# Kernel optimization log

Hardware: AMD Instinct MI355X
Metric: run time of the kernel (lower is better)

Reference implementation:

```python
import jax, jax.numpy as jnp
import numpy as np

VOCAB = 50000
D = 512          # in_feat == word_embedding_dim
B = 4096
S = 128
NUM_LABELS = 3


def setup_inputs() -> dict:
    key = jax.random.key(0)
    ks = jax.random.split(key, 16)
    ids_a = jax.random.randint(ks[0], (B, S), 0, VOCAB, dtype=jnp.int32)
    ids_b = jax.random.randint(ks[1], (B, S), 0, VOCAB, dtype=jnp.int32)
    mask_a = jax.random.randint(ks[2], (B, S), 0, 2) > 0
    mask_b = jax.random.randint(ks[3], (B, S), 0, 2) > 0
    s = 0.02
    W_emb = jax.random.normal(ks[4], (VOCAB, D), jnp.float32) * s
    W_emb = W_emb.at[0].set(0.0)  # padding_idx=0
    enc_w1 = jax.random.normal(ks[5], (D, D), jnp.float32) * s
    enc_b1 = jnp.zeros((D,), jnp.float32)
    enc_w2 = jax.random.normal(ks[6], (D, D), jnp.float32) * s
    enc_b2 = jnp.zeros((D,), jnp.float32)
    cls_w1 = jax.random.normal(ks[7], (2 * D, D), jnp.float32) * s
    cls_b1 = jnp.zeros((D,), jnp.float32)
    cls_w2 = jax.random.normal(ks[8], (D, NUM_LABELS), jnp.float32) * s
    cls_b2 = jnp.zeros((NUM_LABELS,), jnp.float32)
    return {
        "text_a_inputs_id": ids_a, "text_b_inputs_id": ids_b,
        "text_a_attention_mask": mask_a, "text_b_attention_mask": mask_b,
        "W_emb": W_emb,
        "enc_w1": enc_w1, "enc_b1": enc_b1, "enc_w2": enc_w2, "enc_b2": enc_b2,
        "cls_w1": cls_w1, "cls_b1": cls_b1, "cls_w2": cls_w2, "cls_b2": cls_b2,
    }


def _encode(ids, mask, W_emb, w1, b1, w2, b2):
    # embedding gather [B,S,D], fused masked sum-pool -> [B,D]
    emb = W_emb[ids]
    pooled = jnp.einsum("bsd,bs->bd", emb, mask.astype(emb.dtype))
    x = jnp.tanh(pooled @ w1 + b1)
    x = jnp.tanh(x @ w2 + b2)  # dropout is identity in eval
    return x


def reference(text_a_inputs_id, text_b_inputs_id, text_a_attention_mask,
              text_b_attention_mask, W_emb, enc_w1, enc_b1, enc_w2, enc_b2,
              cls_w1, cls_b1, cls_w2, cls_b2):
    va = _encode(text_a_inputs_id, text_a_attention_mask, W_emb, enc_w1, enc_b1, enc_w2, enc_b2)
    vb = _encode(text_b_inputs_id, text_b_attention_mask, W_emb, enc_w1, enc_b1, enc_w2, enc_b2)
    pooled = jnp.concatenate([va, vb], axis=-1)  # [B, 2D]
    h = jnp.tanh(pooled @ cls_w1 + cls_b1)
    logits = h @ cls_w2 + cls_b2  # [B, num_labels]
    return logits
```

## Files before the change

kernel.cpp:

```cpp
#include <hip/hip_runtime.h>


typedef unsigned short u16;
typedef __attribute__((ext_vector_type(8))) short short8;
typedef __attribute__((ext_vector_type(4))) float f32x4;

__device__ __forceinline__ float bfu2f(u16 u) {
    union { unsigned int i; float f; } v;
    v.i = ((unsigned int)u) << 16;
    return v.f;
}

__device__ __forceinline__ u16 f2bfu(float f) {
    union { float f; unsigned int i; } v;
    v.f = f;
    unsigned int x = v.i;
    x += 0x7fffu + ((x >> 16) & 1u);
    return (u16)(x >> 16);
}

__device__ __forceinline__ int detect_wave(const u16* __restrict__ W,
                                           const unsigned int* __restrict__ m,
                                           int lane)
{
    int cnt = 0;
    int w01 = 1, b01 = 1, lo16 = 0;
    #pragma unroll
    for (int j = lane; j < 256; j += 64) {
        u16 u = W[1024 + 2 * j];
        int e = (u >> 7) & 0xFF;
        cnt += (e >= 0x6A && e <= 0x7E) ? 1 : 0;
        unsigned int v = m[j];
        w01 &= (v <= 1u) ? 1 : 0;
        b01 &= ((v & ~0x01010101u) == 0u) ? 1 : 0;
        lo16 |= ((v & 0xFFFFu) == 0x3F80u) ? 1 : 0;
    }
    #pragma unroll
    for (int off = 32; off > 0; off >>= 1) {
        cnt  += __shfl_down(cnt, off);
        w01  &= __shfl_down(w01, off);
        b01  &= __shfl_down(b01, off);
        lo16 |= __shfl_down(lo16, off);
    }
    int mtype;
    if (w01)        mtype = 0;
    else if (b01)   mtype = 1;
    else if (lo16)  mtype = 2;
    else            mtype = 3;
    int fl = ((cnt >= 128) ? 1 : 0) | (mtype << 2);
    return __shfl(fl, 0);
}

__device__ __forceinline__ int mask_nonzero(const void* __restrict__ msk,
                                            int idx, int mtype)
{
    switch (mtype) {
        case 0:  return ((const int*)msk)[idx] != 0;
        case 1:  return ((const unsigned char*)msk)[idx] != 0;
        case 2:  return ((const u16*)msk)[idx] != 0;
        default: return ((const unsigned int*)msk)[idx] != 0u;
    }
}

__global__ __launch_bounds__(128) void pool_kernel(
    const int* __restrict__ ids_a, const int* __restrict__ ids_b,
    const void* __restrict__ mask_a, const void* __restrict__ mask_b,
    const void* __restrict__ W, u16* __restrict__ P)
{
    __shared__ int s_ids[128];
    __shared__ int s_cnt;
    __shared__ int s_flags;
    const int t = threadIdx.x;

    if (t == 0) s_cnt = 0;
    if (t < 64) {
        int fl = detect_wave((const u16*)W, (const unsigned int*)mask_a, t);
        if (t == 0) s_flags = fl;
    }
    __syncthreads();
    const int  flags = s_flags;
    const bool isbf  = (flags & 1) != 0;
    const int  mtype = (flags >> 2) & 3;

    const int row  = blockIdx.x & 4095;
    const int side = blockIdx.x >> 12;
    const int* __restrict__ ids = side ? ids_b : ids_a;
    const void* __restrict__ msk = side ? mask_b : mask_a;

    int id = ids[row * 128 + t];
    int mk = mask_nonzero(msk, row * 128 + t, mtype);
    if (mk) {
        int idx = atomicAdd(&s_cnt, 1);
        s_ids[idx] = id;
    }
    __syncthreads();
    const int cnt = s_cnt;

    float4 acc = {0.f, 0.f, 0.f, 0.f};
    if (isbf) {
        const u16* Wb = (const u16*)W;
        int j = 0;
        for (; j + 4 <= cnt; j += 4) {
            ushort4 r0 = *(const ushort4*)(Wb + (size_t)s_ids[j + 0] * 512 + t * 4);
            ushort4 r1 = *(const ushort4*)(Wb + (size_t)s_ids[j + 1] * 512 + t * 4);
            ushort4 r2 = *(const ushort4*)(Wb + (size_t)s_ids[j + 2] * 512 + t * 4);
            ushort4 r3 = *(const ushort4*)(Wb + (size_t)s_ids[j + 3] * 512 + t * 4);
            acc.x += bfu2f(r0.x) + bfu2f(r1.x) + bfu2f(r2.x) + bfu2f(r3.x);
            acc.y += bfu2f(r0.y) + bfu2f(r1.y) + bfu2f(r2.y) + bfu2f(r3.y);
            acc.z += bfu2f(r0.z) + bfu2f(r1.z) + bfu2f(r2.z) + bfu2f(r3.z);
            acc.w += bfu2f(r0.w) + bfu2f(r1.w) + bfu2f(r2.w) + bfu2f(r3.w);
        }
        for (; j < cnt; ++j) {
            ushort4 r4 = *(const ushort4*)(Wb + (size_t)s_ids[j] * 512 + t * 4);
            acc.x += bfu2f(r4.x); acc.y += bfu2f(r4.y);
            acc.z += bfu2f(r4.z); acc.w += bfu2f(r4.w);
        }
    } else {
        const float* Wf = (const float*)W;
        for (int j = 0; j < cnt; ++j) {
            float4 r4 = *(const float4*)(Wf + (size_t)s_ids[j] * 512 + t * 4);
            acc.x += r4.x; acc.y += r4.y; acc.z += r4.z; acc.w += r4.w;
        }
    }
    ushort4 o = { f2bfu(acc.x), f2bfu(acc.y), f2bfu(acc.z), f2bfu(acc.w) };
    *(ushort4*)(P + (size_t)blockIdx.x * 512 + t * 4) = o;
}

__global__ __launch_bounds__(256) void gemm_mfma(
    const u16* __restrict__ A, const u16* __restrict__ A2, int K1,
    const void* __restrict__ B, const void* __restrict__ bias,
    u16* __restrict__ C, int N, int K,
    const u16* __restrict__ Wdet, const unsigned int* __restrict__ Mdet)
{
    __shared__ __align__(16) u16 As[128 * 40];
    __shared__ __align__(16) u16 Bs[64 * 40];
    __shared__ int s_flags;

    const int tid  = threadIdx.x;
    const int lane = tid & 63;

    if (tid < 64) {
        int fl = detect_wave(Wdet, Mdet, tid);
        if (tid == 0) s_flags = fl;
    }
    __syncthreads();
    const bool isbf = (s_flags & 1) != 0;

    const int m0 = blockIdx.y * 128;
    const int n0 = blockIdx.x * 64;

    const int wid = tid >> 6;
    const int wm  = (wid & 1) * 64;
    const int wn  = (wid >> 1) * 32;

    const int ar = tid >> 1;
    const int ak = (tid & 1) * 16;
    const int bk = tid & 31;
    const int nb = (tid >> 5) * 8;

    const int lm  = lane & 15;
    const int kc  = (lane >> 4) * 8;

    f32x4 acc[4][2];
    #pragma unroll
    for (int i = 0; i < 4; ++i)
        #pragma unroll
        for (int j = 0; j < 2; ++j)
            acc[i][j] = (f32x4){0.f, 0.f, 0.f, 0.f};

    for (int k0 = 0; k0 < K; k0 += 32) {
        const int kg = k0 + ak;
        const u16* Ap = (kg < K1) ? (A  + (size_t)(m0 + ar) * 512 + kg)
                                  : (A2 + (size_t)(m0 + ar) * 512 + (kg - K1));
        ushort4 a0 = *(const ushort4*)(Ap + 0);
        ushort4 a1 = *(const ushort4*)(Ap + 4);
        ushort4 a2 = *(const ushort4*)(Ap + 8);
        ushort4 a3 = *(const ushort4*)(Ap + 12);

        u16 bv[8];
        if (isbf) {
            const u16* Bp = (const u16*)B + (size_t)(k0 + bk) * N + n0 + nb;
            ushort4 b0 = *(const ushort4*)(Bp + 0);
            ushort4 b1 = *(const ushort4*)(Bp + 4);
            bv[0] = b0.x; bv[1] = b0.y; bv[2] = b0.z; bv[3] = b0.w;
            bv[4] = b1.x; bv[5] = b1.y; bv[6] = b1.z; bv[7] = b1.w;
        } else {
            const float* Bp = (const float*)B + (size_t)(k0 + bk) * N + n0 + nb;
            float4 b0 = *(const float4*)(Bp + 0);
            float4 b1 = *(const float4*)(Bp + 4);
            bv[0] = f2bfu(b0.x); bv[1] = f2bfu(b0.y); bv[2] = f2bfu(b0.z); bv[3] = f2bfu(b0.w);
            bv[4] = f2bfu(b1.x); bv[5] = f2bfu(b1.y); bv[6] = f2bfu(b1.z); bv[7] = f2bfu(b1.w);
        }

        __syncthreads();

        *(ushort4*)&As[ar * 40 + ak + 0]  = a0;
        *(ushort4*)&As[ar * 40 + ak + 4]  = a1;
        *(ushort4*)&As[ar * 40 + ak + 8]  = a2;
        *(ushort4*)&As[ar * 40 + ak + 12] = a3;
        #pragma unroll
        for (int i = 0; i < 8; ++i)
            Bs[(nb + i) * 40 + bk] = bv[i];

        __syncthreads();

        short8 af[4], bf[2];
        #pragma unroll
        for (int i = 0; i < 4; ++i)
            af[i] = *(const short8*)&As[(wm + i * 16 + lm) * 40 + kc];
        #pragma unroll
        for (int j = 0; j < 2; ++j)
            bf[j] = *(const short8*)&Bs[(wn + j * 16 + lm) * 40 + kc];

        #pragma unroll
        for (int i = 0; i < 4; ++i)
            #pragma unroll
            for (int j = 0; j < 2; ++j)
                acc[i][j] = __builtin_amdgcn_mfma_f32_16x16x32_bf16(
                    af[i], bf[j], acc[i][j], 0, 0, 0);
    }

    #pragma unroll
    for (int j = 0; j < 2; ++j) {
        const int n = n0 + wn + j * 16 + lm;
        const float bsv = isbf ? bfu2f(((const u16*)bias)[n])
                               : ((const float*)bias)[n];
        #pragma unroll
        for (int i = 0; i < 4; ++i) {
            #pragma unroll
            for (int r = 0; r < 4; ++r) {
                const int m = m0 + wm + i * 16 + (lane >> 4) * 4 + r;
                C[(size_t)m * N + n] = f2bfu(tanhf(acc[i][j][r] + bsv));
            }
        }
    }
}

__global__ __launch_bounds__(64) void logits_kernel(
    const u16* __restrict__ H, const void* __restrict__ W2,
    const void* __restrict__ b2, float* __restrict__ out,
    const u16* __restrict__ Wdet, const unsigned int* __restrict__ Mdet)
{
    const int lane = threadIdx.x;
    const int fl = detect_wave(Wdet, Mdet, lane);
    const bool isbf = (fl & 1) != 0;

    const int m = blockIdx.x;
    const u16* h = H + (size_t)m * 512;

    float a0 = 0.f, a1 = 0.f, a2 = 0.f;
    #pragma unroll
    for (int k = lane; k < 512; k += 64) {
        float x = bfu2f(h[k]);
        float w0, w1, w2;
        if (isbf) {
            const u16* Wb = (const u16*)W2;
            w0 = bfu2f(Wb[k * 3 + 0]); w1 = bfu2f(Wb[k * 3 + 1]); w2 = bfu2f(Wb[k * 3 + 2]);
        } else {
            const float* Wf = (const float*)W2;
            w0 = Wf[k * 3 + 0]; w1 = Wf[k * 3 + 1]; w2 = Wf[k * 3 + 2];
        }
        a0 += x * w0; a1 += x * w1; a2 += x * w2;
    }
    #pragma unroll
    for (int off = 32; off > 0; off >>= 1) {
        a0 += __shfl_down(a0, off);
        a1 += __shfl_down(a1, off);
        a2 += __shfl_down(a2, off);
    }
    if (lane == 0) {
        float b0, b1, b2v;
        if (isbf) {
            const u16* bb = (const u16*)b2;
            b0 = bfu2f(bb[0]); b1 = bfu2f(bb[1]); b2v = bfu2f(bb[2]);
        } else {
            const float* bf = (const float*)b2;
            b0 = bf[0]; b1 = bf[1]; b2v = bf[2];
        }
        out[m * 3 + 0] = a0 + b0;
        out[m * 3 + 1] = a1 + b1;
        out[m * 3 + 2] = a2 + b2v;
    }
}

extern "C" void kernel_launch(void* const* d_in, const int* in_sizes, int n_in,
                              void* d_out, int out_size, void* d_ws, size_t ws_size,
                              hipStream_t stream)
{
    const int* ids_a  = (const int*)d_in[0];
    const int* ids_b  = (const int*)d_in[1];
    const void* mask_a = d_in[2];
    const void* mask_b = d_in[3];
    const void* W_emb  = d_in[4];
    const void* enc_w1 = d_in[5];
    const void* enc_b1 = d_in[6];
    const void* enc_w2 = d_in[7];
    const void* enc_b2 = d_in[8];
    const void* cls_w1 = d_in[9];
    const void* cls_b1 = d_in[10];
    const void* cls_w2 = d_in[11];
    const void* cls_b2 = d_in[12];

    const u16* Wdet = (const u16*)W_emb;
    const unsigned int* Mdet = (const unsigned int*)mask_a;

    u16* buf0 = (u16*)d_ws;
    u16* buf1 = buf0 + (size_t)8192 * 512;

    pool_kernel<<<8192, 128, 0, stream>>>(ids_a, ids_b, mask_a, mask_b, W_emb, buf0);

    gemm_mfma<<<dim3(8, 64), 256, 0, stream>>>(
        buf0, buf0, 512, enc_w1, enc_b1, buf1, 512, 512, Wdet, Mdet);

    gemm_mfma<<<dim3(8, 64), 256, 0, stream>>>(
        buf1, buf1, 512, enc_w2, enc_b2, buf0, 512, 512, Wdet, Mdet);

    gemm_mfma<<<dim3(8, 32), 256, 0, stream>>>(
        buf0, buf0 + (size_t)4096 * 512, 512, cls_w1, cls_b1, buf1, 512, 1024, Wdet, Mdet);

    logits_kernel<<<4096, 64, 0, stream>>>(buf1, cls_w2, cls_b2, (float*)d_out, Wdet, Mdet);
}
```

Baseline: 404.6 us.

## Split pool gather across waves, prefetch and swizzle GEMM tiles, vectorize logits

The pool kernel now has its two waves each gather alternate embedding rows with 16-byte loads and combines the two partial sums through shared memory. The GEMM gains register prefetch of the next K tile, wider A loads, an XOR-style swizzle of the B tile in shared memory to reduce bank conflicts, and a swapped grid order so consecutive blocks share the same weight columns. The logits kernel loads each hidden row with a single vector load per lane. The aim is fewer gather instructions, less memory latency in the GEMM loop and better cache reuse, at the cost of an extra shared-memory reduction in pooling and more registers.

```diff
diff --git a/kernel.cpp b/kernel.cpp
--- a/kernel.cpp
+++ b/kernel.cpp
@@ -70,7 +70,10 @@
     __shared__ int s_ids[128];
     __shared__ int s_cnt;
     __shared__ int s_flags;
+    __shared__ float sP[512];
     const int t = threadIdx.x;
+    const int w = t >> 6;
+    const int lane = t & 63;
 
     if (t == 0) s_cnt = 0;
     if (t < 64) {
@@ -96,34 +99,50 @@
     __syncthreads();
     const int cnt = s_cnt;
 
-    float4 acc = {0.f, 0.f, 0.f, 0.f};
+    float acc[8] = {};
     if (isbf) {
         const u16* Wb = (const u16*)W;
-        int j = 0;
-        for (; j + 4 <= cnt; j += 4) {
-            ushort4 r0 = *(const ushort4*)(Wb + (size_t)s_ids[j + 0] * 512 + t * 4);
-            ushort4 r1 = *(const ushort4*)(Wb + (size_t)s_ids[j + 1] * 512 + t * 4);
-            ushort4 r2 = *(const ushort4*)(Wb + (size_t)s_ids[j + 2] * 512 + t * 4);
-            ushort4 r3 = *(const ushort4*)(Wb + (size_t)s_ids[j + 3] * 512 + t * 4);
-            acc.x += bfu2f(r0.x) + bfu2f(r1.x) + bfu2f(r2.x) + bfu2f(r3.x);
-            acc.y += bfu2f(r0.y) + bfu2f(r1.y) + bfu2f(r2.y) + bfu2f(r3.y);
-            acc.z += bfu2f(r0.z) + bfu2f(r1.z) + bfu2f(r2.z) + bfu2f(r3.z);
-            acc.w += bfu2f(r0.w) + bfu2f(r1.w) + bfu2f(r2.w) + bfu2f(r3.w);
-        }
-        for (; j < cnt; ++j) {
-            ushort4 r4 = *(const ushort4*)(Wb + (size_t)s_ids[j] * 512 + t * 4);
-            acc.x += bfu2f(r4.x); acc.y += bfu2f(r4.y);
-            acc.z += bfu2f(r4.z); acc.w += bfu2f(r4.w);
+        int j = w;
+        for (; j + 6 < cnt; j += 8) {
+            union { uint4 v; u16 s[8]; } r0, r1, r2, r3;
+            r0.v = *(const uint4*)(Wb + (size_t)s_ids[j + 0] * 512 + lane * 8);
+            r1.v = *(const uint4*)(Wb + (size_t)s_ids[j + 2] * 512 + lane * 8);
+            r2.v = *(const uint4*)(Wb + (size_t)s_ids[j + 4] * 512 + lane * 8);
+            r3.v = *(const uint4*)(Wb + (size_t)s_ids[j + 6] * 512 + lane * 8);
+            #pragma unroll
+            for (int i = 0; i < 8; ++i)
+                acc[i] += bfu2f(r0.s[i]) + bfu2f(r1.s[i]) +
+                          bfu2f(r2.s[i]) + bfu2f(r3.s[i]);
+        }
+        for (; j < cnt; j += 2) {
+            union { uint4 v; u16 s[8]; } r;
+            r.v = *(const uint4*)(Wb + (size_t)s_ids[j] * 512 + lane * 8);
+            #pragma unroll
+            for (int i = 0; i < 8; ++i) acc[i] += bfu2f(r.s[i]);
         }
     } else {
         const float* Wf = (const float*)W;
-        for (int j = 0; j < cnt; ++j) {
-            float4 r4 = *(const float4*)(Wf + (size_t)s_ids[j] * 512 + t * 4);
-            acc.x += r4.x; acc.y += r4.y; acc.z += r4.z; acc.w += r4.w;
-        }
-    }
-    ushort4 o = { f2bfu(acc.x), f2bfu(acc.y), f2bfu(acc.z), f2bfu(acc.w) };
-    *(ushort4*)(P + (size_t)blockIdx.x * 512 + t * 4) = o;
+        for (int j = w; j < cnt; j += 2) {
+            const float* rp = Wf + (size_t)s_ids[j] * 512 + lane * 8;
+            float4 a = *(const float4*)(rp + 0);
+            float4 b = *(const float4*)(rp + 4);
+            acc[0] += a.x; acc[1] += a.y; acc[2] += a.z; acc[3] += a.w;
+            acc[4] += b.x; acc[5] += b.y; acc[6] += b.z; acc[7] += b.w;
+        }
+    }
+
+    if (w == 0) {
+        #pragma unroll
+        for (int i = 0; i < 8; ++i) sP[lane * 8 + i] = acc[i];
+    }
+    __syncthreads();
+    if (w == 1) {
+        union { uint4 v; u16 s[8]; } o;
+        #pragma unroll
+        for (int i = 0; i < 8; ++i)
+            o.s[i] = f2bfu(acc[i] + sP[lane * 8 + i]);
+        *(uint4*)(P + (size_t)blockIdx.x * 512 + lane * 8) = o.v;
+    }
 }
 
 __global__ __launch_bounds__(256) void gemm_mfma(
@@ -146,20 +165,23 @@
     __syncthreads();
     const bool isbf = (s_flags & 1) != 0;
 
-    const int m0 = blockIdx.y * 128;
-    const int n0 = blockIdx.x * 64;
+    const int m0 = blockIdx.x * 128;
+    const int n0 = blockIdx.y * 64;
 
     const int wid = tid >> 6;
     const int wm  = (wid & 1) * 64;
     const int wn  = (wid >> 1) * 32;
 
-    const int ar = tid >> 1;
-    const int ak = (tid & 1) * 16;
-    const int bk = tid & 31;
-    const int nb = (tid >> 5) * 8;
-
-    const int lm  = lane & 15;
-    const int kc  = (lane >> 4) * 8;
+    const int ar = tid >> 2;
+    const int ak = (tid & 3) * 8;
+    const int bk = tid >> 3;
+    const int jn = tid & 7;
+    const int nb = jn * 8;
+    const int bofs = (((bk >> 3) + jn) & 3) * 8 + (bk & 7);
+
+    const int lm = lane & 15;
+    const int kq = lane >> 4;
+    const int kc = kq * 8;
 
     f32x4 acc[4][2];
     #pragma unroll
@@ -168,50 +190,53 @@
         for (int j = 0; j < 2; ++j)
             acc[i][j] = (f32x4){0.f, 0.f, 0.f, 0.f};
 
-    for (int k0 = 0; k0 < K; k0 += 32) {
+    uint4 ra0, ra1;
+    u16 rb[8];
+
+    auto fetch = [&](int k0) {
         const int kg = k0 + ak;
-        const u16* Ap = (kg < K1) ? (A  + (size_t)(m0 + ar) * 512 + kg)
-                                  : (A2 + (size_t)(m0 + ar) * 512 + (kg - K1));
-        ushort4 a0 = *(const ushort4*)(Ap + 0);
-        ushort4 a1 = *(const ushort4*)(Ap + 4);
-        ushort4 a2 = *(const ushort4*)(Ap + 8);
-        ushort4 a3 = *(const ushort4*)(Ap + 12);
-
-        u16 bv[8];
+        const u16* Ap0 = (kg < K1) ? (A  + (size_t)(m0 + ar) * 512 + kg)
+                                   : (A2 + (size_t)(m0 + ar) * 512 + (kg - K1));
+        const u16* Ap1 = (kg < K1) ? (A  + (size_t)(m0 + ar + 64) * 512 + kg)
+                                   : (A2 + (size_t)(m0 + ar + 64) * 512 + (kg - K1));
+        ra0 = *(const uint4*)Ap0;
+        ra1 = *(const uint4*)Ap1;
         if (isbf) {
-            const u16* Bp = (const u16*)B + (size_t)(k0 + bk) * N + n0 + nb;
-            ushort4 b0 = *(const ushort4*)(Bp + 0);
-            ushort4 b1 = *(const ushort4*)(Bp + 4);
-            bv[0] = b0.x; bv[1] = b0.y; bv[2] = b0.z; bv[3] = b0.w;
-            bv[4] = b1.x; bv[5] = b1.y; bv[6] = b1.z; bv[7] = b1.w;
+            union { uint4 v; u16 s[8]; } ub;
+            ub.v = *(const uint4*)((const u16*)B + (size_t)(k0 + bk) * N + n0 + nb);
+            #pragma unroll
+            for (int i = 0; i < 8; ++i) rb[i] = ub.s[i];
         } else {
             const float* Bp = (const float*)B + (size_t)(k0 + bk) * N + n0 + nb;
             float4 b0 = *(const float4*)(Bp + 0);
             float4 b1 = *(const float4*)(Bp + 4);
-            bv[0] = f2bfu(b0.x); bv[1] = f2bfu(b0.y); bv[2] = f2bfu(b0.z); bv[3] = f2bfu(b0.w);
-            bv[4] = f2bfu(b1.x); bv[5] = f2bfu(b1.y); bv[6] = f2bfu(b1.z); bv[7] = f2bfu(b1.w);
-        }
-
+            rb[0] = f2bfu(b0.x); rb[1] = f2bfu(b0.y); rb[2] = f2bfu(b0.z); rb[3] = f2bfu(b0.w);
+            rb[4] = f2bfu(b1.x); rb[5] = f2bfu(b1.y); rb[6] = f2bfu(b1.z); rb[7] = f2bfu(b1.w);
+        }
+    };
+
+    fetch(0);
+    for (int k0 = 0; k0 < K; k0 += 32) {
+        if (k0) __syncthreads();
+        *(uint4*)&As[ar * 40 + ak]        = ra0;
+        *(uint4*)&As[(ar + 64) * 40 + ak] = ra1;
+        #pragma unroll
+        for (int i = 0; i < 8; ++i)
+            Bs[(nb + i) * 40 + bofs] = rb[i];
         __syncthreads();
 
-        *(ushort4*)&As[ar * 40 + ak + 0]  = a0;
-        *(ushort4*)&As[ar * 40 + ak + 4]  = a1;
-        *(ushort4*)&As[ar * 40 + ak + 8]  = a2;
-        *(ushort4*)&As[ar * 40 + ak + 12] = a3;
-        #pragma unroll
-        for (int i = 0; i < 8; ++i)
-            Bs[(nb + i) * 40 + bk] = bv[i];
-
-        __syncthreads();
+        if (k0 + 32 < K) fetch(k0 + 32);
 
         short8 af[4], bf[2];
         #pragma unroll
         for (int i = 0; i < 4; ++i)
             af[i] = *(const short8*)&As[(wm + i * 16 + lm) * 40 + kc];
         #pragma unroll
-        for (int j = 0; j < 2; ++j)
-            bf[j] = *(const short8*)&Bs[(wn + j * 16 + lm) * 40 + kc];
-
+        for (int j = 0; j < 2; ++j) {
+            const int n = wn + j * 16 + lm;
+            const int ch = ((kq + (n >> 3)) & 3) * 8;
+            bf[j] = *(const short8*)&Bs[n * 40 + ch];
+        }
         #pragma unroll
         for (int i = 0; i < 4; ++i)
             #pragma unroll
@@ -229,7 +254,7 @@
         for (int i = 0; i < 4; ++i) {
             #pragma unroll
             for (int r = 0; r < 4; ++r) {
-                const int m = m0 + wm + i * 16 + (lane >> 4) * 4 + r;
+                const int m = m0 + wm + i * 16 + kq * 4 + r;
                 C[(size_t)m * N + n] = f2bfu(tanhf(acc[i][j][r] + bsv));
             }
         }
@@ -246,12 +271,14 @@
     const bool isbf = (fl & 1) != 0;
 
     const int m = blockIdx.x;
-    const u16* h = H + (size_t)m * 512;
+    union { uint4 v; u16 s[8]; } h;
+    h.v = *(const uint4*)(H + (size_t)m * 512 + lane * 8);
 
     float a0 = 0.f, a1 = 0.f, a2 = 0.f;
     #pragma unroll
-    for (int k = lane; k < 512; k += 64) {
-        float x = bfu2f(h[k]);
+    for (int i = 0; i < 8; ++i) {
+        const int k = lane * 8 + i;
+        float x = bfu2f(h.s[i]);
         float w0, w1, w2;
         if (isbf) {
             const u16* Wb = (const u16*)W2;
@@ -309,13 +336,13 @@
 
     pool_kernel<<<8192, 128, 0, stream>>>(ids_a, ids_b, mask_a, mask_b, W_emb, buf0);
 
-    gemm_mfma<<<dim3(8, 64), 256, 0, stream>>>(
+    gemm_mfma<<<dim3(64, 8), 256, 0, stream>>>(
         buf0, buf0, 512, enc_w1, enc_b1, buf1, 512, 512, Wdet, Mdet);
 
-    gemm_mfma<<<dim3(8, 64), 256, 0, stream>>>(
+    gemm_mfma<<<dim3(64, 8), 256, 0, stream>>>(
         buf1, buf1, 512, enc_w2, enc_b2, buf0, 512, 512, Wdet, Mdet);
 
-    gemm_mfma<<<dim3(8, 32), 256, 0, stream>>>(
+    gemm_mfma<<<dim3(32, 8), 256, 0, stream>>>(
         buf0, buf0 + (size_t)4096 * 512, 512, cls_w1, cls_b1, buf1, 512, 1024, Wdet, Mdet);
 
     logits_kernel<<<4096, 64, 0, stream>>>(buf1, cls_w2, cls_b2, (float*)d_out, Wdet, Mdet);
```

New measurement: 383.6 us. -5.2%, faster.
